# Kernel optimization log

Measured on AMD Instinct MI355X. Metric: run time of the kernel, lower is better.

## Reference

```python
import jax, jax.numpy as jnp
import numpy as np

B, FH, N, TIN = 8, 8, 2048, 5      # batch(time for LSTM), f_length, nodes, in_length
H1, H2 = 32, 64                    # traj_linear_hidden, lstm_encoder_size
NEG = -9e15

def setup_inputs() -> dict:
    key = jax.random.key(0)
    ks = jax.random.split(key, 12)
    s = lambda k, shape, fan: jax.random.normal(k, shape, jnp.float32) * (1.0 / np.sqrt(fan))
    return {
        "hist": jax.random.normal(ks[0], (B, FH, N, TIN), jnp.float32),
        "adj": jax.random.randint(ks[1], (B, 2, N, N), 0, 2, jnp.int32),
        "W1": s(ks[2], (H1, TIN * FH), TIN * FH),
        "b1": jnp.zeros((H1,), jnp.float32),
        "W_ih": s(ks[3], (4 * H2, H1), H1),
        "W_hh": s(ks[4], (4 * H2, H2), H2),
        "b_ih": jnp.zeros((4 * H2,), jnp.float32),
        "b_hh": jnp.zeros((4 * H2,), jnp.float32),
        "Wg": s(ks[5], (H2, H2), H2),
        "a_src": s(ks[6], (H2,), H2),
        "a_dst": s(ks[7], (H2,), H2),
    }

def _lstm(x, W_ih, W_hh, b_ih, b_hh):
    # x: [T, Nb, H1] (torch nn.LSTM seq-first); gate order i,f,g,o
    Nb = x.shape[1]
    h0 = jnp.zeros((Nb, H2), x.dtype)
    c0 = jnp.zeros((Nb, H2), x.dtype)
    def step(carry, xt):
        h, c = carry
        g = xt @ W_ih.T + b_ih + h @ W_hh.T + b_hh        # [Nb, 4*H2]
        i, f, gg, o = jnp.split(g, 4, axis=-1)
        c = jax.nn.sigmoid(f) * c + jax.nn.sigmoid(i) * jnp.tanh(gg)
        h = jax.nn.sigmoid(o) * jnp.tanh(c)
        return (h, c), h
    _, hs = jax.lax.scan(step, (h0, c0), x)
    return hs                                              # [T, Nb, H2]

def reference(hist, adj, W1, b1, W_ih, W_hh, b_ih, b_hh, Wg, a_src, a_dst):
    # hist.permute(0,2,3,1).flatten(2,3) -> [B, N, TIN*FH]
    x = jnp.transpose(hist, (0, 2, 3, 1)).reshape(B, N, TIN * FH)
    h1 = jax.nn.elu(x @ W1.T + b1)                         # [B, N, H1]
    hs = _lstm(h1, W_ih, W_hh, b_ih, b_hh)                 # [B, N, H2]
    # GAT over adj[:, -1]
    A = adj[:, -1, :, :] > 0                               # [B, N, N]
    Wh = hs @ Wg                                           # [B, N, H2]
    e = jax.nn.leaky_relu(
        (Wh @ a_src)[:, :, None] + (Wh @ a_dst)[:, None, :], 0.2)
    e = jnp.where(A, e, NEG)
    alpha = jax.nn.softmax(e, axis=-1)                     # [B, N, N]
    out = jax.nn.elu(jnp.einsum("bij,bjd->bid", alpha, Wh))
    return out
```

## Files before the change

### kernel.cpp

```cpp
#include <hip/hip_runtime.h>
#include <hip/hip_bf16.h>
#include <math.h>

#define BB 8
#define FH 8
#define NN 2048
#define TIN 5
#define H1 32
#define H2 64

typedef const void* cvp;
typedef __attribute__((ext_vector_type(8))) short short8;
typedef __attribute__((ext_vector_type(4))) float floatx4;

__device__ __forceinline__ float ldx(cvp p, int i, int bf) {
  if (bf) return __bfloat162float(((const __hip_bfloat16*)p)[i]);
  return ((const float*)p)[i];
}

__device__ __forceinline__ float4 ld4(cvp p, int i, int bf) {
  if (bf) {
    const __hip_bfloat162* q = (const __hip_bfloat162*)p;
    float2 a = __bfloat1622float2(q[(i >> 1)]);
    float2 b = __bfloat1622float2(q[(i >> 1) + 1]);
    return make_float4(a.x, a.y, b.x, b.y);
  }
  return ((const float4*)p)[i >> 2];
}

__device__ __forceinline__ float sigf(float x) {
  return 1.f / (1.f + __expf(-x));
}

__global__ void k_detect(const unsigned int* __restrict__ w, int* __restrict__ flag) {
  __shared__ int cnt;
  if (threadIdx.x == 0) cnt = 0;
  __syncthreads();
  int local = 0;
  for (int i = threadIdx.x; i < 1024; i += 256) {
    unsigned e = (w[i] >> 7) & 0xFFu;
    local += (e >= 100u && e <= 150u) ? 1 : 0;
  }
  atomicAdd(&cnt, local);
  __syncthreads();
  if (threadIdx.x == 0) *flag = (cnt > 700) ? 1 : 0;
}

__global__ __launch_bounds__(256, 2) void k_lstm(
    cvp hist, cvp W1, cvp b1, cvp W_ih, cvp W_hh, cvp b_ih, cvp b_hh,
    float* __restrict__ hs, const int* __restrict__ flagp) {
  __shared__ __align__(16) float xh[4][96];
  __shared__ float gbuf[4][256];
  __shared__ float W1s[H1][41];
  __shared__ float b1s[H1];
  __shared__ float xstage[4][40];
  int bf = *flagp;
  int tid = threadIdx.x;
  int w = tid >> 6, lane = tid & 63;
  int g = (w << 6) + lane;
  int n0 = blockIdx.x << 2;
  int node_w = n0 + w;

  for (int i = tid; i < H1 * 40; i += 256) W1s[i / 40][i % 40] = ldx(W1, i, bf);
  if (tid < H1) b1s[tid] = ldx(b1, tid, bf);

  float wreg[96];
#pragma unroll
  for (int kq = 0; kq < 8; ++kq) {
    float4 v = ld4(W_ih, g * 32 + (kq << 2), bf);
    wreg[(kq << 2) + 0] = v.x; wreg[(kq << 2) + 1] = v.y;
    wreg[(kq << 2) + 2] = v.z; wreg[(kq << 2) + 3] = v.w;
  }
#pragma unroll
  for (int kq = 0; kq < 16; ++kq) {
    float4 v = ld4(W_hh, g * 64 + (kq << 2), bf);
    wreg[32 + (kq << 2) + 0] = v.x; wreg[32 + (kq << 2) + 1] = v.y;
    wreg[32 + (kq << 2) + 2] = v.z; wreg[32 + (kq << 2) + 3] = v.w;
  }
  float bias = ldx(b_ih, g, bf) + ldx(b_hh, g, bf);

  xh[w][32 + lane] = 0.f;
  float c = 0.f;

  for (int t = 0; t < BB; ++t) {
    if (tid < 160) {
      int nd = tid / 40, r = tid % 40;
      int ti = r >> 3, f = r & 7;
      xstage[nd][r] = ldx(hist, ((t * FH + f) * NN + n0 + nd) * TIN + ti, bf);
    }
    __syncthreads();
    if (tid < 128) {
      int nd = tid >> 5, k = tid & 31;
      float acc = b1s[k];
#pragma unroll
      for (int j = 0; j < 40; ++j) acc += W1s[k][j] * xstage[nd][j];
      xh[nd][k] = (acc > 0.f) ? acc : expm1f(acc);
    }
    __syncthreads();
    float acc[4] = {bias, bias, bias, bias};
    const float4* xq0 = (const float4*)xh[0];
    const float4* xq1 = (const float4*)xh[1];
    const float4* xq2 = (const float4*)xh[2];
    const float4* xq3 = (const float4*)xh[3];
#pragma unroll
    for (int kq = 0; kq < 24; ++kq) {
      float w0 = wreg[(kq << 2) + 0], w1 = wreg[(kq << 2) + 1];
      float w2 = wreg[(kq << 2) + 2], w3 = wreg[(kq << 2) + 3];
      float4 v0 = xq0[kq], v1 = xq1[kq], v2 = xq2[kq], v3 = xq3[kq];
      acc[0] += w0 * v0.x + w1 * v0.y + w2 * v0.z + w3 * v0.w;
      acc[1] += w0 * v1.x + w1 * v1.y + w2 * v1.z + w3 * v1.w;
      acc[2] += w0 * v2.x + w1 * v2.y + w2 * v2.z + w3 * v2.w;
      acc[3] += w0 * v3.x + w1 * v3.y + w2 * v3.z + w3 * v3.w;
    }
#pragma unroll
    for (int nd = 0; nd < 4; ++nd) gbuf[nd][g] = acc[nd];
    __syncthreads();
    float gi = gbuf[w][lane];
    float gf = gbuf[w][64 + lane];
    float gg = gbuf[w][128 + lane];
    float go = gbuf[w][192 + lane];
    c = sigf(gf) * c + sigf(gi) * tanhf(gg);
    float h = sigf(go) * tanhf(c);
    xh[w][32 + lane] = h;
    hs[((t * NN + node_w) * H2) + lane] = h;
    __syncthreads();
  }
}

__global__ __launch_bounds__(256) void k_gatprep(
    const float* __restrict__ hs, cvp Wg, cvp a_src, cvp a_dst,
    __hip_bfloat16* __restrict__ WhFr, float* __restrict__ sv,
    float* __restrict__ dv, const int* __restrict__ flagp) {
  __shared__ float wg[H2 * H2];
  __shared__ float tile[32][H2 + 1];
  int bf = *flagp;
  int tid = threadIdx.x;
  for (int i = tid; i < H2 * H2; i += 256) wg[i] = ldx(Wg, i, bf);
  __syncthreads();
  int wave = tid >> 6, lane = tid & 63;
  int b = blockIdx.x >> 6;
  int jt = blockIdx.x & 63;
  int j0 = jt << 5;
  float as = ldx(a_src, lane, bf);
  float ad = ldx(a_dst, lane, bf);
#pragma unroll
  for (int rr = 0; rr < 8; ++rr) {
    int jl = (wave << 3) + rr;
    int row = b * NN + j0 + jl;
    float hreg = hs[row * H2 + lane];
    float acc = 0.f;
#pragma unroll
    for (int k = 0; k < H2; ++k)
      acc += __shfl(hreg, k, 64) * wg[(k << 6) + lane];
    tile[jl][lane] = acc;
    float s = acc * as, d = acc * ad;
#pragma unroll
    for (int off = 32; off > 0; off >>= 1) {
      s += __shfl_xor(s, off, 64);
      d += __shfl_xor(d, off, 64);
    }
    if (lane == 0) { sv[row] = s; dv[row] = d; }
  }
  __syncthreads();
  int nt = tid >> 6, l = tid & 63;
  int q = l >> 4, m = l & 15;
  float v[8];
#pragma unroll
  for (int jj = 0; jj < 8; ++jj)
    v[jj] = tile[(q << 3) + jj][(nt << 4) + m];
  short8 fr;
#pragma unroll
  for (int p = 0; p < 4; ++p)
    ((__hip_bfloat162*)&fr)[p] =
        __float22bfloat162_rn(make_float2(v[2 * p], v[2 * p + 1]));
  size_t off = ((size_t)(b * 64 + jt) * 4 + nt) * 64 + l;
  ((short8*)WhFr)[off] = fr;
}

__global__ __launch_bounds__(256, 3) void k_gat(
    const int* __restrict__ adj, const __hip_bfloat16* __restrict__ WhFr,
    const float* __restrict__ sv, const float* __restrict__ dv,
    void* __restrict__ out, const int* __restrict__ flagp) {
  __shared__ __align__(16) float dv_s[NN];
  __shared__ unsigned int msk[16 * 65];
  __shared__ floatx4 abuf[3][5][64];
  int bf = *flagp;
  int tid = threadIdx.x;
  int w = tid >> 6, lane = tid & 63;
  int b = blockIdx.x >> 7;
  int i0 = (blockIdx.x & 127) << 4;
  int q = lane >> 4, m = lane & 15;

  for (int j = tid; j < NN; j += 256) dv_s[j] = dv[b * NN + j];
  const int* adjb = adj + ((size_t)(b * 2 + 1) * NN + i0) * NN;
#pragma unroll
  for (int rr = 0; rr < 4; ++rr) {
    int row = (w << 2) + rr;
    const int* ar = adjb + (size_t)row * NN;
#pragma unroll 8
    for (int it = 0; it < 32; ++it) {
      int v = ar[(it << 6) + lane];
      unsigned long long bal = __ballot(v != 0);
      if (lane == 0) {
        msk[row * 65 + (it << 1)] = (unsigned)bal;
        msk[row * 65 + (it << 1) + 1] = (unsigned)(bal >> 32);
      }
    }
  }
  float sva = sv[b * NN + i0 + m];
  __syncthreads();

  short8 ones;
#pragma unroll
  for (int p = 0; p < 8; ++p) ones[p] = (short)0x3F80;

  const short8* base = ((const short8*)WhFr) + (size_t)b * 16384 + lane;
  int ksb = w << 4, kse = ksb + 16;
  floatx4 acc0 = {0.f, 0.f, 0.f, 0.f};
  floatx4 acc1 = acc0, acc2 = acc0, acc3 = acc0, accS = acc0;

  for (int ks = ksb; ks < kse; ++ks) {
    const short8* b_ks = base + (size_t)ks * 256;
    short8 b0 = b_ks[0];
    short8 b1 = b_ks[64];
    short8 b2 = b_ks[128];
    short8 b3 = b_ks[192];
    unsigned mword = msk[m * 65 + ks];
    float4 d0 = *(const float4*)&dv_s[(ks << 5) + (q << 3)];
    float4 d1 = *(const float4*)&dv_s[(ks << 5) + (q << 3) + 4];
    float dd[8] = {d0.x, d0.y, d0.z, d0.w, d1.x, d1.y, d1.z, d1.w};
    float pv[8];
#pragma unroll
    for (int jj = 0; jj < 8; ++jj) {
      float t = sva + dd[jj];
      float e = __expf(fmaxf(t, 0.2f * t));
      pv[jj] = ((mword >> ((q << 3) + jj)) & 1u) ? e : 0.f;
    }
    short8 afr;
#pragma unroll
    for (int p2 = 0; p2 < 4; ++p2)
      ((__hip_bfloat162*)&afr)[p2] =
          __float22bfloat162_rn(make_float2(pv[2 * p2], pv[2 * p2 + 1]));
    acc0 = __builtin_amdgcn_mfma_f32_16x16x32_bf16(afr, b0, acc0, 0, 0, 0);
    acc1 = __builtin_amdgcn_mfma_f32_16x16x32_bf16(afr, b1, acc1, 0, 0, 0);
    acc2 = __builtin_amdgcn_mfma_f32_16x16x32_bf16(afr, b2, acc2, 0, 0, 0);
    acc3 = __builtin_amdgcn_mfma_f32_16x16x32_bf16(afr, b3, acc3, 0, 0, 0);
    accS = __builtin_amdgcn_mfma_f32_16x16x32_bf16(afr, ones, accS, 0, 0, 0);
  }
  if (w > 0) {
    abuf[w - 1][0][lane] = acc0;
    abuf[w - 1][1][lane] = acc1;
    abuf[w - 1][2][lane] = acc2;
    abuf[w - 1][3][lane] = acc3;
    abuf[w - 1][4][lane] = accS;
  }
  __syncthreads();
  if (w != 0) return;
#pragma unroll
  for (int ww = 0; ww < 3; ++ww) {
    acc0 += abuf[ww][0][lane];
    acc1 += abuf[ww][1][lane];
    acc2 += abuf[ww][2][lane];
    acc3 += abuf[ww][3][lane];
    accS += abuf[ww][4][lane];
  }
  floatx4 accs[4] = {acc0, acc1, acc2, acc3};
  float inv[4];
#pragma unroll
  for (int r = 0; r < 4; ++r) inv[r] = 1.f / accS[r];
  if (bf) {
    __hip_bfloat16* o = (__hip_bfloat16*)out;
#pragma unroll
    for (int nt = 0; nt < 4; ++nt)
#pragma unroll
      for (int r = 0; r < 4; ++r) {
        float v = accs[nt][r] * inv[r];
        v = (v > 0.f) ? v : expm1f(v);
        int row = i0 + (q << 2) + r;
        o[((size_t)b * NN + row) * H2 + (nt << 4) + m] = __float2bfloat16(v);
      }
  } else {
    float* o = (float*)out;
#pragma unroll
    for (int nt = 0; nt < 4; ++nt)
#pragma unroll
      for (int r = 0; r < 4; ++r) {
        float v = accs[nt][r] * inv[r];
        v = (v > 0.f) ? v : expm1f(v);
        int row = i0 + (q << 2) + r;
        o[((size_t)b * NN + row) * H2 + (nt << 4) + m] = v;
      }
  }
}

extern "C" void kernel_launch(void* const* d_in, const int* in_sizes, int n_in,
                              void* d_out, int out_size, void* d_ws, size_t ws_size,
                              hipStream_t stream) {
  (void)in_sizes; (void)n_in; (void)out_size; (void)ws_size;
  cvp hist  = d_in[0];
  const int* adj = (const int*)d_in[1];
  cvp W1    = d_in[2];
  cvp b1    = d_in[3];
  cvp W_ih  = d_in[4];
  cvp W_hh  = d_in[5];
  cvp b_ih  = d_in[6];
  cvp b_hh  = d_in[7];
  cvp Wg    = d_in[8];
  cvp a_src = d_in[9];
  cvp a_dst = d_in[10];

  float* ws  = (float*)d_ws;
  float* hs  = ws;
  __hip_bfloat16* WhFr = (__hip_bfloat16*)(hs + BB * NN * H2);
  float* sv  = hs + BB * NN * H2 + 524288;
  float* dv  = sv + BB * NN;
  int* flag  = (int*)(dv + BB * NN);

  k_detect<<<1, 256, 0, stream>>>((const unsigned int*)W_ih, flag);
  k_lstm<<<512, 256, 0, stream>>>(hist, W1, b1, W_ih, W_hh, b_ih, b_hh, hs, flag);
  k_gatprep<<<512, 256, 0, stream>>>(hs, Wg, a_src, a_dst, WhFr, sv, dv, flag);
  k_gat<<<1024, 256, 0, stream>>>(adj, WhFr, sv, dv, d_out, flag);
}
```

Before: 467.0 us.

## Inline dtype detection per kernel and vectorize adjacency mask build with int4 loads

Result: faster. 418.1 us (-10.5%).

```diff
diff --git a/kernel.cpp b/kernel.cpp
--- a/kernel.cpp
+++ b/kernel.cpp
@@ -32,29 +32,22 @@
   return 1.f / (1.f + __expf(-x));
 }
 
-__global__ void k_detect(const unsigned int* __restrict__ w, int* __restrict__ flag) {
-  __shared__ int cnt;
-  if (threadIdx.x == 0) cnt = 0;
-  __syncthreads();
-  int local = 0;
-  for (int i = threadIdx.x; i < 1024; i += 256) {
-    unsigned e = (w[i] >> 7) & 0xFFu;
-    local += (e >= 100u && e <= 150u) ? 1 : 0;
-  }
-  atomicAdd(&cnt, local);
-  __syncthreads();
-  if (threadIdx.x == 0) *flag = (cnt > 700) ? 1 : 0;
+__device__ __forceinline__ int detect_bf(cvp wih) {
+  unsigned word = ((const unsigned*)wih)[threadIdx.x & 63];
+  unsigned e = (word >> 7) & 0xFFu;
+  unsigned long long bal = __ballot(e >= 100u && e <= 150u);
+  return __popcll(bal) > 44;
 }
 
 __global__ __launch_bounds__(256, 2) void k_lstm(
     cvp hist, cvp W1, cvp b1, cvp W_ih, cvp W_hh, cvp b_ih, cvp b_hh,
-    float* __restrict__ hs, const int* __restrict__ flagp) {
+    float* __restrict__ hs) {
   __shared__ __align__(16) float xh[4][96];
   __shared__ float gbuf[4][256];
   __shared__ float W1s[H1][41];
   __shared__ float b1s[H1];
   __shared__ float xstage[4][40];
-  int bf = *flagp;
+  int bf = detect_bf(W_ih);
   int tid = threadIdx.x;
   int w = tid >> 6, lane = tid & 63;
   int g = (w << 6) + lane;
@@ -128,12 +121,12 @@
 }
 
 __global__ __launch_bounds__(256) void k_gatprep(
-    const float* __restrict__ hs, cvp Wg, cvp a_src, cvp a_dst,
+    const float* __restrict__ hs, cvp Wg, cvp a_src, cvp a_dst, cvp W_ih,
     __hip_bfloat16* __restrict__ WhFr, float* __restrict__ sv,
-    float* __restrict__ dv, const int* __restrict__ flagp) {
+    float* __restrict__ dv) {
   __shared__ float wg[H2 * H2];
   __shared__ float tile[32][H2 + 1];
-  int bf = *flagp;
+  int bf = detect_bf(W_ih);
   int tid = threadIdx.x;
   for (int i = tid; i < H2 * H2; i += 256) wg[i] = ldx(Wg, i, bf);
   __syncthreads();
@@ -177,37 +170,35 @@
   ((short8*)WhFr)[off] = fr;
 }
 
-__global__ __launch_bounds__(256, 3) void k_gat(
+__global__ __launch_bounds__(256, 4) void k_gat(
     const int* __restrict__ adj, const __hip_bfloat16* __restrict__ WhFr,
     const float* __restrict__ sv, const float* __restrict__ dv,
-    void* __restrict__ out, const int* __restrict__ flagp) {
+    void* __restrict__ out, cvp W_ih) {
   __shared__ __align__(16) float dv_s[NN];
   __shared__ unsigned int msk[16 * 65];
   __shared__ floatx4 abuf[3][5][64];
-  int bf = *flagp;
+  int bf = detect_bf(W_ih);
   int tid = threadIdx.x;
   int w = tid >> 6, lane = tid & 63;
   int b = blockIdx.x >> 7;
   int i0 = (blockIdx.x & 127) << 4;
   int q = lane >> 4, m = lane & 15;
 
+  for (int j = tid; j < 16 * 65; j += 256) msk[j] = 0u;
   for (int j = tid; j < NN; j += 256) dv_s[j] = dv[b * NN + j];
-  const int* adjb = adj + ((size_t)(b * 2 + 1) * NN + i0) * NN;
-#pragma unroll
-  for (int rr = 0; rr < 4; ++rr) {
-    int row = (w << 2) + rr;
-    const int* ar = adjb + (size_t)row * NN;
-#pragma unroll 8
-    for (int it = 0; it < 32; ++it) {
-      int v = ar[(it << 6) + lane];
-      unsigned long long bal = __ballot(v != 0);
-      if (lane == 0) {
-        msk[row * 65 + (it << 1)] = (unsigned)bal;
-        msk[row * 65 + (it << 1) + 1] = (unsigned)(bal >> 32);
-      }
-    }
-  }
   float sva = sv[b * NN + i0 + m];
+  __syncthreads();
+
+  const int4* adj4 = (const int4*)(adj + ((size_t)(b * 2 + 1) * NN + i0) * NN);
+#pragma unroll 16
+  for (int gi = 0; gi < 32; ++gi) {
+    int g = (w << 5) + gi;
+    int row = g >> 3, seg = g & 7;
+    int4 v = adj4[(size_t)row * 512 + (seg << 6) + lane];
+    unsigned nib = (v.x != 0 ? 1u : 0u) | (v.y != 0 ? 2u : 0u) |
+                   (v.z != 0 ? 4u : 0u) | (v.w != 0 ? 8u : 0u);
+    atomicOr(&msk[row * 65 + (seg << 3) + (lane >> 3)], nib << ((lane & 7) << 2));
+  }
   __syncthreads();
 
   short8 ones;
@@ -314,10 +305,8 @@
   __hip_bfloat16* WhFr = (__hip_bfloat16*)(hs + BB * NN * H2);
   float* sv  = hs + BB * NN * H2 + 524288;
   float* dv  = sv + BB * NN;
-  int* flag  = (int*)(dv + BB * NN);
-
-  k_detect<<<1, 256, 0, stream>>>((const unsigned int*)W_ih, flag);
-  k_lstm<<<512, 256, 0, stream>>>(hist, W1, b1, W_ih, W_hh, b_ih, b_hh, hs, flag);
-  k_gatprep<<<512, 256, 0, stream>>>(hs, Wg, a_src, a_dst, WhFr, sv, dv, flag);
-  k_gat<<<1024, 256, 0, stream>>>(adj, WhFr, sv, dv, d_out, flag);
-}
+
+  k_lstm<<<512, 256, 0, stream>>>(hist, W1, b1, W_ih, W_hh, b_ih, b_hh, hs);
+  k_gatprep<<<512, 256, 0, stream>>>(hs, Wg, a_src, a_dst, W_ih, WhFr, sv, dv);
+  k_gat<<<1024, 256, 0, stream>>>(adj, WhFr, sv, dv, d_out, W_ih);
+}
```
